# Kernel optimization log

Measured on AMD Instinct MI355X. Metric: run time of the kernel, lower is better.

The kernel has to match this reference:

```python
import math
import jax, jax.numpy as jnp
import numpy as np

FACTOR = 5
N_HEADS = 8


def setup_inputs() -> dict:
    key = jax.random.key(0)
    ks = jax.random.split(key, 9)
    B, S, D = 4, 8192, 512
    s = 0.02
    x = jax.random.normal(ks[0], (B, S, D), jnp.float32)
    Wq = jax.random.normal(ks[1], (D, D), jnp.float32) * s
    bq = jax.random.normal(ks[2], (D,), jnp.float32) * s
    Wk = jax.random.normal(ks[3], (D, D), jnp.float32) * s
    bk = jax.random.normal(ks[4], (D,), jnp.float32) * s
    Wv = jax.random.normal(ks[5], (D, D), jnp.float32) * s
    bv = jax.random.normal(ks[6], (D,), jnp.float32) * s
    Wo = jax.random.normal(ks[7], (D, D), jnp.float32) * s
    bo = jax.random.normal(ks[8], (D,), jnp.float32) * s
    return {"x": x, "Wq": Wq, "bq": bq, "Wk": Wk, "bk": bk,
            "Wv": Wv, "bv": bv, "Wo": Wo, "bo": bo}


def reference(x, Wq, bq, Wk, bk, Wv, bv, Wo, bo):
    B, S, D = x.shape
    H = N_HEADS
    hd = D // H
    scale = hd ** -0.5

    def proj(W, b):
        # [B,S,D] -> [B,H,S,hd]
        return (x @ W + b).reshape(B, S, H, hd).transpose(0, 2, 1, 3)

    q = proj(Wq, bq)
    k = proj(Wk, bk)
    v = proj(Wv, bv)

    # number of "active" queries: O(log S)
    sampled = max(1, min(S, int(FACTOR * math.log(S + 1))))

    sparsity = jnp.sum(q * q, axis=-1)                    # [B,H,S]
    top_idx = jax.lax.top_k(sparsity, sampled)[1]         # [B,H,u]

    sel_q = jnp.take_along_axis(q, top_idx[..., None], axis=2)  # [B,H,u,hd]
    scores = jnp.einsum('bhud,bhsd->bhus', sel_q, k) * scale     # [B,H,u,S]
    attn = jax.nn.softmax(scores, axis=-1)
    sel_ctx = jnp.einsum('bhus,bhsd->bhud', attn, v)             # [B,H,u,hd]

    # default context = mean of values; overwrite rows of selected queries
    ctx = jnp.broadcast_to(v.mean(axis=2, keepdims=True), (B, H, S, hd))
    bi = jnp.arange(B)[:, None, None]
    hi = jnp.arange(H)[None, :, None]
    ctx = ctx.at[bi, hi, top_idx].set(sel_ctx)                   # scatter [B,H,S,hd]

    ctx = ctx.transpose(0, 2, 1, 3).reshape(B, S, D)
    return ctx @ Wo + bo
```

## Files before the change

### kernel.cpp

```cpp
#include <hip/hip_runtime.h>
#include <hip/hip_fp16.h>
#include <math.h>

#define B_ 4
#define S_ 8192
#define D_ 512
#define H_ 8
#define U_ 45
#define NCHUNK 32

typedef unsigned short ushortT;
typedef __attribute__((ext_vector_type(8))) _Float16 half8;
typedef __attribute__((ext_vector_type(4))) float f32x4;

__device__ __forceinline__ ushortT f2h(float f) {
    return __half_as_ushort(__float2half(f));
}
__device__ __forceinline__ float h2f(ushortT u) {
    return __half2float(__ushort_as_half(u));
}

__device__ __forceinline__ void gload_lds16(const ushortT* g, ushortT* l) {
    __builtin_amdgcn_global_load_lds(
        (const __attribute__((address_space(1))) void*)g,
        (__attribute__((address_space(3))) void*)l,
        16, 0, 0);
}

__global__ __launch_bounds__(256) void prep_kernel(
    const float* __restrict__ X, ushortT* __restrict__ Xf,
    const float* __restrict__ Wq, const float* __restrict__ Wk,
    const float* __restrict__ Wv,
    ushortT* __restrict__ WqT, ushortT* __restrict__ WkT,
    ushortT* __restrict__ WvT,
    float* __restrict__ vsum, float* __restrict__ outbase)
{
    __shared__ float t[32][33];
    const int bx = blockIdx.x;
    if (bx < 8192) {
        if (bx == 0) {
            float4 z = {0.f, 0.f, 0.f, 0.f};
            *(float4*)&vsum[threadIdx.x * 8]        = z;
            *(float4*)&vsum[threadIdx.x * 8 + 4]    = z;
            *(float4*)&outbase[threadIdx.x * 8]     = z;
            *(float4*)&outbase[threadIdx.x * 8 + 4] = z;
        }
        size_t i = ((size_t)bx * 256 + threadIdx.x) * 8;
        float4 a = *(const float4*)(X + i);
        float4 b = *(const float4*)(X + i + 4);
        *(ushort4*)(Xf + i)     = make_ushort4(f2h(a.x), f2h(a.y), f2h(a.z), f2h(a.w));
        *(ushort4*)(Xf + i + 4) = make_ushort4(f2h(b.x), f2h(b.y), f2h(b.z), f2h(b.w));
    } else {
        const int idx = bx - 8192;
        const int z = idx >> 8, rem = idx & 255;
        const int r0 = (rem >> 4) * 32, c0 = (rem & 15) * 32;
        const float* W = (z == 0) ? Wq : (z == 1) ? Wk : Wv;
        ushortT* O = (z == 0) ? WqT : (z == 1) ? WkT : WvT;
        const int tx = threadIdx.x & 31, ty4 = (threadIdx.x >> 5) * 4;
#pragma unroll
        for (int i = 0; i < 4; ++i)
            t[ty4 + i][tx] = W[(size_t)(r0 + ty4 + i) * 512 + c0 + tx];
        __syncthreads();
#pragma unroll
        for (int i = 0; i < 4; ++i)
            O[(size_t)(c0 + ty4 + i) * 512 + r0 + tx] = f2h(t[tx][ty4 + i]);
    }
}

__global__ __launch_bounds__(512, 2) void qkv_mfma(
    const ushortT* __restrict__ Xf,
    const ushortT* __restrict__ WqT, const ushortT* __restrict__ WkT,
    const ushortT* __restrict__ WvT,
    const float* __restrict__ bq, const float* __restrict__ bk,
    const float* __restrict__ bv,
    ushortT* __restrict__ Kbuf, ushortT* __restrict__ VT,
    float* __restrict__ sparsity, float* __restrict__ vsum)
{
    __shared__ ushortT lds[3 * 128 * 64];

    const int tid  = threadIdx.x;
    const int w    = tid >> 6, lane = tid & 63;
    const int quad = lane >> 4, c16 = lane & 15;
    const bool fusedQK = (blockIdx.y < 4);
    const int stream = w >> 2;
    const int aw   = fusedQK ? ((w >> 1) & 1) : (w >> 1);
    const int bw   = w & 1;
    const int m0   = blockIdx.x * 128;
    const int n0   = fusedQK ? (blockIdx.y * 128) : ((blockIdx.y - 4) * 256);

    const int srowL = lane >> 3;
    const int slc   = (((lane & 7) - (srowL & 7)) & 7) * 8;
    const int rrot  = c16 & 7;

    const ushortT* Brd = fusedQK ? (lds + 8192 + stream * 8192) : (lds + 16384);
    const int awBase = aw * 64;
    const int bwBase = bw * 64;

    f32x4 acc[4][4];
#pragma unroll
    for (int i = 0; i < 4; ++i)
#pragma unroll
        for (int j = 0; j < 4; ++j) acc[i][j] = (f32x4){0.f, 0.f, 0.f, 0.f};

    for (int k0 = 0; k0 < 512; k0 += 64) {
        __syncthreads();
        if (fusedQK) {
#pragma unroll
            for (int c = 0; c < 2; ++c) {
                const int R  = c * 64 + w * 8 + srowL;
                const int lb = c * 4096 + w * 512;
                gload_lds16(Xf  + (size_t)(m0 + R) * 512 + k0 + slc, lds + lb);
                gload_lds16(WqT + (size_t)(n0 + R) * 512 + k0 + slc, lds + 8192 + lb);
                gload_lds16(WkT + (size_t)(n0 + R) * 512 + k0 + slc, lds + 16384 + lb);
            }
        } else {
#pragma unroll
            for (int c = 0; c < 4; ++c) {
                const int R = c * 64 + w * 8 + srowL;
                gload_lds16(WvT + (size_t)(n0 + R) * 512 + k0 + slc,
                            lds + c * 4096 + w * 512);
            }
#pragma unroll
            for (int c = 0; c < 2; ++c) {
                const int R = c * 64 + w * 8 + srowL;
                gload_lds16(Xf + (size_t)(m0 + R) * 512 + k0 + slc,
                            lds + 16384 + c * 4096 + w * 512);
            }
        }
        __syncthreads();
#pragma unroll
        for (int kk = 0; kk < 2; ++kk) {
            const int phk = (((kk * 4 + quad) + rrot) & 7) * 8;
            half8 af[4], bf[4];
#pragma unroll
            for (int i = 0; i < 4; ++i) {
                af[i] = *(const half8*)&lds[(awBase + i * 16 + c16) * 64 + phk];
                bf[i] = *(const half8*)&Brd[(bwBase + i * 16 + c16) * 64 + phk];
            }
#pragma unroll
            for (int i = 0; i < 4; ++i)
#pragma unroll
                for (int j = 0; j < 4; ++j)
                    acc[i][j] = __builtin_amdgcn_mfma_f32_16x16x32_f16(af[i], bf[j], acc[i][j], 0, 0, 0);
        }
    }

    const int b = m0 >> 13;
    if (fusedQK && stream == 0) {
        const int head = (n0 + bw * 64) >> 6;
        float bb[4];
#pragma unroll
        for (int j = 0; j < 4; ++j) bb[j] = bq[n0 + bw * 64 + j * 16 + c16];
#pragma unroll
        for (int i = 0; i < 4; ++i)
#pragma unroll
            for (int r = 0; r < 4; ++r) {
                const int s = (m0 & 8191) + awBase + i * 16 + quad * 4 + r;
                float p = 0.f;
#pragma unroll
                for (int j = 0; j < 4; ++j) {
                    float v = acc[i][j][r] + bb[j];
                    p = fmaf(v, v, p);
                }
                p += __shfl_xor(p, 1);
                p += __shfl_xor(p, 2);
                p += __shfl_xor(p, 4);
                p += __shfl_xor(p, 8);
                if (c16 == 0)
                    sparsity[((size_t)b * H_ + head) * S_ + s] = p;
            }
    } else if (fusedQK) {
        const int head = (n0 + bw * 64) >> 6;
        float bb[4];
#pragma unroll
        for (int j = 0; j < 4; ++j) bb[j] = bk[n0 + bw * 64 + j * 16 + c16];
        ushortT* kbase = Kbuf + ((size_t)(b * 8 + head) * 8192) * 64;
#pragma unroll
        for (int i = 0; i < 4; ++i)
#pragma unroll
            for (int r = 0; r < 4; ++r) {
                const int s = (m0 & 8191) + awBase + i * 16 + quad * 4 + r;
#pragma unroll
                for (int j = 0; j < 4; ++j)
                    kbase[(size_t)s * 64 + j * 16 + c16] = f2h(acc[i][j][r] + bb[j]);
            }
    } else {
        const int sbase = (m0 & 8191) + bwBase;
#pragma unroll
        for (int i = 0; i < 4; ++i)
#pragma unroll
            for (int r = 0; r < 4; ++r) {
                const int dcol = n0 + awBase + i * 16 + quad * 4 + r;
                const int head = dcol >> 6, dd = dcol & 63;
                const float biasv = bv[dcol];
                ushortT* vrow = VT + ((size_t)(b * 8 + head) * 64 + dd) * 8192;
                float vsa = 0.f;
#pragma unroll
                for (int j = 0; j < 4; ++j) {
                    float v = acc[i][j][r] + biasv;
                    vrow[sbase + j * 16 + c16] = f2h(v);
                    vsa += v;
                }
                vsa += __shfl_xor(vsa, 1);
                vsa += __shfl_xor(vsa, 2);
                vsa += __shfl_xor(vsa, 4);
                vsa += __shfl_xor(vsa, 8);
                if (c16 == 0) atomicAdd(&vsum[b * 512 + dcol], vsa);
            }
    }
}

__global__ __launch_bounds__(256) void topk_kernel(
    const float* __restrict__ sparsity, int* __restrict__ topidx,
    const float* __restrict__ vsum, const float* __restrict__ Wo,
    const float* __restrict__ bo, float* __restrict__ outbase,
    const ushortT* __restrict__ Xf, const ushortT* __restrict__ WqT,
    const float* __restrict__ bq, ushortT* __restrict__ selQ)
{
    __shared__ __align__(16) char smem[49920];
    unsigned* vals        = (unsigned*)smem;
    unsigned (*hist)[256] = (unsigned (*)[256])(smem + 32768);
    int* ssum             = (int*)(smem + 40960);
    int* eqidx            = (int*)(smem + 41984);
    ushortT* selX         = (ushortT*)smem;
    __shared__ unsigned prefix_s;
    __shared__ int need_s;
    __shared__ int cnt_gt_s, cnt_eq_s;
    const int tid = threadIdx.x;

    if (blockIdx.x >= 32) {
        const int idx = blockIdx.x - 32;
        const int b = idx >> 3, ks = (idx & 7) >> 1, dh = idx & 1;
        const int d = dh * 256 + tid;
        float acc = (ks == 0) ? bo[d] : 0.f;
        const int r0 = ks * 128;
        for (int r = r0; r < r0 + 128; ++r) {
            float mv = vsum[b * 512 + r] * (1.0f / S_);
            acc = fmaf(mv, Wo[(size_t)r * 512 + d], acc);
        }
        atomicAdd(&outbase[b * 512 + d], acc);
        return;
    }

    const int bh = blockIdx.x;
    const unsigned* sp = (const unsigned*)(sparsity + (size_t)bh * S_);
    for (int i = tid; i < S_; i += 256) vals[i] = sp[i];

    unsigned prefix = 0;
    int need = U_;
    const int rep = tid & 7;
    for (int level = 0; level < 4; ++level) {
        const int shift = 24 - level * 8;
#pragma unroll
        for (int r = 0; r < 8; ++r) hist[r][tid] = 0;
        __syncthreads();
        const unsigned pmask = (level == 0) ? 0u : (0xFFFFFFFFu << (shift + 8));
        for (int i = tid; i < S_; i += 256) {
            unsigned v = vals[i];
            if ((v & pmask) == prefix)
                atomicAdd(&hist[rep][(v >> shift) & 255], 1u);
        }
        __syncthreads();
        int bs = 0;
#pragma unroll
        for (int r = 0; r < 8; ++r) bs += (int)hist[r][tid];
        ssum[tid] = bs;
        __syncthreads();
        for (int off = 1; off < 256; off <<= 1) {
            int add = (tid + off < 256) ? ssum[tid + off] : 0;
            __syncthreads();
            ssum[tid] += add;
            __syncthreads();
        }
        int snext = (tid == 255) ? 0 : ssum[tid + 1];
        if (ssum[tid] >= need && snext < need) {
            prefix_s = prefix | ((unsigned)tid << shift);
            need_s = need - snext;
        }
        __syncthreads();
        prefix = prefix_s;
        need = need_s;
        __syncthreads();
    }
    const unsigned T = prefix;
    if (tid == 0) { cnt_gt_s = 0; cnt_eq_s = 0; }
    __syncthreads();
    for (int i = tid; i < S_; i += 256) {
        unsigned v = vals[i];
        if (v > T) {
            int p = atomicAdd(&cnt_gt_s, 1);
            topidx[bh * U_ + p] = i;
        } else if (v == T) {
            int p = atomicAdd(&cnt_eq_s, 1);
            if (p < 64) eqidx[p] = i;
        }
    }
    __syncthreads();
    if (tid == 0) {
        int rem = U_ - cnt_gt_s;
        int n = cnt_eq_s < 64 ? cnt_eq_s : 64;
        for (int a = 0; a < rem; ++a) {
            int best = 1 << 30, bj = 0;
            for (int j = 0; j < n; ++j)
                if (eqidx[j] < best) { best = eqidx[j]; bj = j; }
            topidx[bh * U_ + cnt_gt_s + a] = best;
            eqidx[bj] = 1 << 30;
        }
    }
    __syncthreads();

    const int b = bh >> 3, h = bh & 7;
    for (int i = tid; i < 48 * 64; i += 256) {
        const int row = i >> 6, ch = i & 63;
        half8 v;
#pragma unroll
        for (int z = 0; z < 8; ++z) v[z] = (_Float16)0.0f;
        if (row < U_) {
            const int s = topidx[bh * U_ + row];
            v = *(const half8*)&Xf[((size_t)b * 8192 + s) * 512 + ch * 8];
        }
        *(half8*)&selX[row * 520 + ch * 8] = v;
    }
    __syncthreads();

    const int w = tid >> 6, lane = tid & 63;
    const int quad = lane >> 4, c16 = lane & 15;
    f32x4 qacc[3];
#pragma unroll
    for (int mt = 0; mt < 3; ++mt) qacc[mt] = (f32x4){0.f, 0.f, 0.f, 0.f};
    const ushortT* brow = WqT + (size_t)(h * 64 + w * 16 + c16) * 512;
    for (int k0 = 0; k0 < 512; k0 += 32) {
        half8 bf = *(const half8*)&brow[k0 + quad * 8];
#pragma unroll
        for (int mt = 0; mt < 3; ++mt) {
            half8 af = *(const half8*)&selX[(mt * 16 + c16) * 520 + k0 + quad * 8];
            qacc[mt] = __builtin_amdgcn_mfma_f32_16x16x32_f16(af, bf, qacc[mt], 0, 0, 0);
        }
    }
    const float bb = bq[h * 64 + w * 16 + c16];
    ushortT* oq = selQ + (size_t)bh * 48 * 64 + (w * 16 + c16);
#pragma unroll
    for (int mt = 0; mt < 3; ++mt)
#pragma unroll
        for (int r = 0; r < 4; ++r) {
            const int m = mt * 16 + quad * 4 + r;
            float v = (m < U_) ? (qacc[mt][r] + bb) * 0.125f : 0.f;
            oq[(size_t)m * 64] = f2h(v);
        }
}

__global__ __launch_bounds__(256, 2) void attn_mfma(
    const ushortT* __restrict__ selQ, const ushortT* __restrict__ Kbuf,
    const ushortT* __restrict__ VT,
    float* __restrict__ pl, float* __restrict__ pacc)
{
    __shared__ float sc[48 * 132];

    const int tid = threadIdx.x;
    const int w = tid >> 6, lane = tid & 63;
    const int quad = lane >> 4, c16 = lane & 15;
    const int bh = blockIdx.y;
    const int s_base = blockIdx.x * (S_ / NCHUNK);

    f32x4 O[3];
#pragma unroll
    for (int mt = 0; mt < 3; ++mt) O[mt] = (f32x4){0.f, 0.f, 0.f, 0.f};
    float lacc[12];
#pragma unroll
    for (int qi = 0; qi < 12; ++qi) lacc[qi] = 0.f;

    const ushortT* sq = selQ + (size_t)bh * 48 * 64;
    half8 qa[3][2];
#pragma unroll
    for (int mt = 0; mt < 3; ++mt)
#pragma unroll
        for (int kk = 0; kk < 2; ++kk)
            qa[mt][kk] = *(const half8*)&sq[(mt * 16 + c16) * 64 + kk * 32 + quad * 8];

    const ushortT* kb  = Kbuf + (size_t)bh * 8192 * 64;
    const ushortT* vtb = VT + ((size_t)bh * 64 + w * 16 + c16) * 8192;

    half8 kf0[2][2], kf1[2][2], vb0[4], vb1[4];
#pragma unroll
    for (int nt2 = 0; nt2 < 2; ++nt2)
#pragma unroll
        for (int kk = 0; kk < 2; ++kk) {
            kf0[nt2][kk] = *(const half8*)&kb[
                (size_t)(s_base + w * 32 + nt2 * 16 + c16) * 64 + kk * 32 + quad * 8];
            kf1[nt2][kk] = *(const half8*)&kb[
                (size_t)(s_base + 128 + w * 32 + nt2 * 16 + c16) * 64 + kk * 32 + quad * 8];
        }
#pragma unroll
    for (int kk = 0; kk < 4; ++kk) {
        vb0[kk] = *(const half8*)&vtb[s_base + kk * 32 + quad * 8];
        vb1[kk] = *(const half8*)&vtb[s_base + 128 + kk * 32 + quad * 8];
    }

    auto chunk = [&](const half8 (&kf)[2][2], const half8 (&vb)[4]) {
        f32x4 sacc[3][2];
#pragma unroll
        for (int mt = 0; mt < 3; ++mt)
#pragma unroll
            for (int nt2 = 0; nt2 < 2; ++nt2) {
                sacc[mt][nt2] = (f32x4){0.f, 0.f, 0.f, 0.f};
#pragma unroll
                for (int kk = 0; kk < 2; ++kk)
                    sacc[mt][nt2] = __builtin_amdgcn_mfma_f32_16x16x32_f16(
                        qa[mt][kk], kf[nt2][kk], sacc[mt][nt2], 0, 0, 0);
            }
#pragma unroll
        for (int mt = 0; mt < 3; ++mt)
#pragma unroll
            for (int nt2 = 0; nt2 < 2; ++nt2)
#pragma unroll
                for (int r = 0; r < 4; ++r)
                    sc[(mt * 16 + quad * 4 + r) * 132 + w * 32 + nt2 * 16 + c16] =
                        sacc[mt][nt2][r];
        __syncthreads();

#pragma unroll
        for (int qi = 0; qi < 12; ++qi) {
            const int q = w * 12 + qi;
            float x0 = sc[q * 132 + lane];
            float x1 = sc[q * 132 + 64 + lane];
            ushortT u0 = f2h(__expf(x0));
            ushortT u1 = f2h(__expf(x1));
            lacc[qi] += h2f(u0) + h2f(u1);
            ushortT* pr = (ushortT*)&sc[q * 132];
            pr[lane] = u0;
            pr[lane + 64] = u1;
        }
        __syncthreads();

#pragma unroll
        for (int mt = 0; mt < 3; ++mt)
#pragma unroll
            for (int kk = 0; kk < 4; ++kk) {
                half8 pa = *(const half8*)((const ushortT*)sc +
                    (size_t)(mt * 16 + c16) * 264 + kk * 32 + quad * 8);
                O[mt] = __builtin_amdgcn_mfma_f32_16x16x32_f16(pa, vb[kk], O[mt], 0, 0, 0);
            }
        __syncthreads();
    };

    chunk(kf0, vb0);
    chunk(kf1, vb1);

#pragma unroll
    for (int mt = 0; mt < 3; ++mt)
#pragma unroll
        for (int r = 0; r < 4; ++r) {
            const int q = mt * 16 + quad * 4 + r;
            if (q < U_)
                pacc[(((size_t)bh * NCHUNK + blockIdx.x) * U_ + q) * 64 + w * 16 + c16] =
                    O[mt][r];
        }
#pragma unroll
    for (int qi = 0; qi < 12; ++qi) {
        const int q = w * 12 + qi;
        float ssum = lacc[qi];
#pragma unroll
        for (int off = 1; off < 64; off <<= 1) ssum += __shfl_xor(ssum, off);
        if (lane == 0 && q < U_)
            pl[((size_t)bh * NCHUNK + blockIdx.x) * U_ + q] = ssum;
    }
}

__global__ __launch_bounds__(256) void fill_kernel(
    const float* __restrict__ outbase, float* __restrict__ out)
{
    size_t gid = (size_t)blockIdx.x * 256 + threadIdx.x;
    size_t e0 = gid * 4;
    int b = (int)(e0 >> 22);
    int col = (int)(e0 & 511);
    float4 v = *(const float4*)&outbase[b * 512 + col];
    *(float4*)&out[e0] = v;
}

__global__ __launch_bounds__(512) void corr_out_kernel(
    const float* __restrict__ pl, const float* __restrict__ pacc,
    const float* __restrict__ vsum, const float* __restrict__ Wo,
    const int* __restrict__ topidx, float* __restrict__ out)
{
    __shared__ float redA[8][64];
    __shared__ float redL[8];
    __shared__ float corrS[64];
    const int q = blockIdx.x, bh = blockIdx.y;
    const int b = bh >> 3, h = bh & 7, tid = threadIdx.x;
    const int g = tid >> 6, lane = tid & 63;

    float a = 0.f, L = 0.f;
    for (int c = g; c < NCHUNK; c += 8) {
        a += pacc[(((size_t)bh * NCHUNK + c) * U_ + q) * 64 + lane];
        if (lane == 0) L += pl[((size_t)bh * NCHUNK + c) * U_ + q];
    }
    redA[g][lane] = a;
    if (lane == 0) redL[g] = L;
    __syncthreads();
    if (tid < 64) {
        float asum = 0.f, Lsum = 0.f;
#pragma unroll
        for (int gg = 0; gg < 8; ++gg) { asum += redA[gg][tid]; Lsum += redL[gg]; }
        corrS[tid] = asum / Lsum - vsum[b * 512 + h * 64 + tid] * (1.0f / S_);
    }
    __syncthreads();
    const int s = topidx[bh * U_ + q];
    const int d = tid;
    float delta = 0.f;
#pragma unroll
    for (int r = 0; r < 64; ++r)
        delta = fmaf(corrS[r], Wo[(size_t)(h * 64 + r) * 512 + d], delta);
    atomicAdd(&out[((size_t)b * S_ + s) * 512 + d], delta);
}

extern "C" void kernel_launch(void* const* d_in, const int* in_sizes, int n_in,
                              void* d_out, int out_size, void* d_ws, size_t ws_size,
                              hipStream_t stream)
{
    const float* X  = (const float*)d_in[0];
    const float* Wq = (const float*)d_in[1];
    const float* bq = (const float*)d_in[2];
    const float* Wk = (const float*)d_in[3];
    const float* bk = (const float*)d_in[4];
    const float* Wv = (const float*)d_in[5];
    const float* bv = (const float*)d_in[6];
    const float* Wo = (const float*)d_in[7];
    const float* bo = (const float*)d_in[8];
    float* out = (float*)d_out;

    char* ws = (char*)d_ws;
    size_t off = 0;
    auto alloc = [&](size_t bytes) {
        void* p = ws + off;
        off = (off + bytes + 255) & ~(size_t)255;
        return p;
    };
    ushortT* Xf   = (ushortT*)alloc((size_t)B_ * S_ * D_ * 2);
    ushortT* Kbuf = (ushortT*)alloc((size_t)B_ * S_ * D_ * 2);
    ushortT* VT   = (ushortT*)alloc((size_t)B_ * S_ * D_ * 2);
    ushortT* WqT  = (ushortT*)alloc((size_t)D_ * D_ * 2);
    ushortT* WkT  = (ushortT*)alloc((size_t)D_ * D_ * 2);
    ushortT* WvT  = (ushortT*)alloc((size_t)D_ * D_ * 2);
    ushortT* selQ = (ushortT*)alloc((size_t)B_ * H_ * 48 * 64 * 2);
    float* sparsity = (float*)alloc((size_t)B_ * H_ * S_ * 4);
    int*   topidx   = (int*)alloc((size_t)B_ * H_ * U_ * 4);
    float* pl       = (float*)alloc((size_t)B_ * H_ * NCHUNK * U_ * 4);
    float* pacc     = (float*)alloc((size_t)B_ * H_ * NCHUNK * U_ * 64 * 4);
    float* vsum     = (float*)alloc((size_t)B_ * 512 * 4);
    float* outbase  = (float*)alloc((size_t)B_ * 512 * 4);

    prep_kernel<<<8960, 256, 0, stream>>>(X, Xf, Wq, Wk, Wv, WqT, WkT, WvT,
                                          vsum, outbase);
    qkv_mfma<<<dim3(256, 6), 512, 0, stream>>>(Xf, WqT, WkT, WvT,
                                               bq, bk, bv, Kbuf, VT,
                                               sparsity, vsum);
    topk_kernel<<<64, 256, 0, stream>>>(sparsity, topidx, vsum, Wo, bo, outbase,
                                        Xf, WqT, bq, selQ);
    attn_mfma<<<dim3(NCHUNK, B_ * H_), 256, 0, stream>>>(selQ, Kbuf, VT,
                                                         pl, pacc);
    fill_kernel<<<(B_ * S_ * D_ / 4 + 255) / 256, 256, 0, stream>>>(outbase, out);
    corr_out_kernel<<<dim3(U_, B_ * H_), 512, 0, stream>>>(pl, pacc, vsum, Wo,
                                                           topidx, out);
}
```

Baseline: 277.2 us.

## Share X tile across Q and K accumulators in fused QK projection blocks

Fused Q/K blocks now cover 256 rows of X, and each wave keeps both Q and K accumulators, so one A-fragment load feeds two MFMAs. Before, Q and K were handled by separate wave groups that each re-read the same X tile. The grid is unchanged, so half of the QK blocks exit at once. Register pressure doubles to two 4x4 accumulator sets per wave, and LDS grows to four tiles, which may lower occupancy and cause spills under launch_bounds(512,2).

```diff
diff --git a/kernel.cpp b/kernel.cpp
--- a/kernel.cpp
+++ b/kernel.cpp
@@ -76,91 +76,89 @@
     ushortT* __restrict__ Kbuf, ushortT* __restrict__ VT,
     float* __restrict__ sparsity, float* __restrict__ vsum)
 {
-    __shared__ ushortT lds[3 * 128 * 64];
+    __shared__ ushortT lds[4 * 128 * 64];
 
     const int tid  = threadIdx.x;
     const int w    = tid >> 6, lane = tid & 63;
     const int quad = lane >> 4, c16 = lane & 15;
     const bool fusedQK = (blockIdx.y < 4);
-    const int stream = w >> 2;
-    const int aw   = fusedQK ? ((w >> 1) & 1) : (w >> 1);
-    const int bw   = w & 1;
-    const int m0   = blockIdx.x * 128;
-    const int n0   = fusedQK ? (blockIdx.y * 128) : ((blockIdx.y - 4) * 256);
-
     const int srowL = lane >> 3;
     const int slc   = (((lane & 7) - (srowL & 7)) & 7) * 8;
     const int rrot  = c16 & 7;
 
-    const ushortT* Brd = fusedQK ? (lds + 8192 + stream * 8192) : (lds + 16384);
-    const int awBase = aw * 64;
-    const int bwBase = bw * 64;
-
-    f32x4 acc[4][4];
-#pragma unroll
-    for (int i = 0; i < 4; ++i)
-#pragma unroll
-        for (int j = 0; j < 4; ++j) acc[i][j] = (f32x4){0.f, 0.f, 0.f, 0.f};
-
-    for (int k0 = 0; k0 < 512; k0 += 64) {
-        __syncthreads();
-        if (fusedQK) {
+    if (fusedQK) {
+        if (blockIdx.x >= 128) return;
+        const int m0 = blockIdx.x * 256;
+        const int n0 = blockIdx.y * 128;
+        const int wr = w >> 1, wc = w & 1;
+
+        f32x4 accQ[4][4], accK[4][4];
+#pragma unroll
+        for (int i = 0; i < 4; ++i)
+#pragma unroll
+            for (int j = 0; j < 4; ++j) {
+                accQ[i][j] = (f32x4){0.f, 0.f, 0.f, 0.f};
+                accK[i][j] = (f32x4){0.f, 0.f, 0.f, 0.f};
+            }
+
+        for (int k0 = 0; k0 < 512; k0 += 64) {
+            __syncthreads();
+#pragma unroll
+            for (int c = 0; c < 4; ++c) {
+                const int R = c * 64 + w * 8 + srowL;
+                gload_lds16(Xf + (size_t)(m0 + R) * 512 + k0 + slc,
+                            lds + c * 4096 + w * 512);
+            }
 #pragma unroll
             for (int c = 0; c < 2; ++c) {
                 const int R  = c * 64 + w * 8 + srowL;
                 const int lb = c * 4096 + w * 512;
-                gload_lds16(Xf  + (size_t)(m0 + R) * 512 + k0 + slc, lds + lb);
-                gload_lds16(WqT + (size_t)(n0 + R) * 512 + k0 + slc, lds + 8192 + lb);
-                gload_lds16(WkT + (size_t)(n0 + R) * 512 + k0 + slc, lds + 16384 + lb);
-            }
-        } else {
-#pragma unroll
-            for (int c = 0; c < 4; ++c) {
-                const int R = c * 64 + w * 8 + srowL;
-                gload_lds16(WvT + (size_t)(n0 + R) * 512 + k0 + slc,
-                            lds + c * 4096 + w * 512);
-            }
-#pragma unroll
-            for (int c = 0; c < 2; ++c) {
-                const int R = c * 64 + w * 8 + srowL;
-                gload_lds16(Xf + (size_t)(m0 + R) * 512 + k0 + slc,
-                            lds + 16384 + c * 4096 + w * 512);
-            }
-        }
-        __syncthreads();
-#pragma unroll
-        for (int kk = 0; kk < 2; ++kk) {
-            const int phk = (((kk * 4 + quad) + rrot) & 7) * 8;
-            half8 af[4], bf[4];
-#pragma unroll
-            for (int i = 0; i < 4; ++i) {
-                af[i] = *(const half8*)&lds[(awBase + i * 16 + c16) * 64 + phk];
-                bf[i] = *(const half8*)&Brd[(bwBase + i * 16 + c16) * 64 + phk];
-            }
-#pragma unroll
-            for (int i = 0; i < 4; ++i)
-#pragma unroll
-                for (int j = 0; j < 4; ++j)
-                    acc[i][j] = __builtin_amdgcn_mfma_f32_16x16x32_f16(af[i], bf[j], acc[i][j], 0, 0, 0);
-        }
-    }
-
-    const int b = m0 >> 13;
-    if (fusedQK && stream == 0) {
-        const int head = (n0 + bw * 64) >> 6;
-        float bb[4];
-#pragma unroll
-        for (int j = 0; j < 4; ++j) bb[j] = bq[n0 + bw * 64 + j * 16 + c16];
+                gload_lds16(WqT + (size_t)(n0 + R) * 512 + k0 + slc,
+                            lds + 16384 + lb);
+                gload_lds16(WkT + (size_t)(n0 + R) * 512 + k0 + slc,
+                            lds + 24576 + lb);
+            }
+            __syncthreads();
+#pragma unroll
+            for (int kk = 0; kk < 2; ++kk) {
+                const int phk = (((kk * 4 + quad) + rrot) & 7) * 8;
+                half8 af[4], bq8[4], bk8[4];
+#pragma unroll
+                for (int i = 0; i < 4; ++i) {
+                    af[i]  = *(const half8*)&lds[(wr * 64 + i * 16 + c16) * 64 + phk];
+                    bq8[i] = *(const half8*)&lds[16384 + (wc * 64 + i * 16 + c16) * 64 + phk];
+                    bk8[i] = *(const half8*)&lds[24576 + (wc * 64 + i * 16 + c16) * 64 + phk];
+                }
+#pragma unroll
+                for (int i = 0; i < 4; ++i)
+#pragma unroll
+                    for (int j = 0; j < 4; ++j) {
+                        accQ[i][j] = __builtin_amdgcn_mfma_f32_16x16x32_f16(af[i], bq8[j], accQ[i][j], 0, 0, 0);
+                        accK[i][j] = __builtin_amdgcn_mfma_f32_16x16x32_f16(af[i], bk8[j], accK[i][j], 0, 0, 0);
+                    }
+            }
+        }
+
+        const int b = m0 >> 13;
+        const int head = (n0 + wc * 64) >> 6;
+        float bbq[4], bbk[4];
+#pragma unroll
+        for (int j = 0; j < 4; ++j) {
+            bbq[j] = bq[n0 + wc * 64 + j * 16 + c16];
+            bbk[j] = bk[n0 + wc * 64 + j * 16 + c16];
+        }
+        ushortT* kbase = Kbuf + ((size_t)(b * 8 + head) * 8192) * 64;
 #pragma unroll
         for (int i = 0; i < 4; ++i)
 #pragma unroll
             for (int r = 0; r < 4; ++r) {
-                const int s = (m0 & 8191) + awBase + i * 16 + quad * 4 + r;
+                const int s = (m0 & 8191) + wr * 64 + i * 16 + quad * 4 + r;
                 float p = 0.f;
 #pragma unroll
                 for (int j = 0; j < 4; ++j) {
-                    float v = acc[i][j][r] + bb[j];
+                    float v = accQ[i][j][r] + bbq[j];
                     p = fmaf(v, v, p);
+                    kbase[(size_t)s * 64 + j * 16 + c16] = f2h(accK[i][j][r] + bbk[j]);
                 }
                 p += __shfl_xor(p, 1);
                 p += __shfl_xor(p, 2);
@@ -169,45 +167,78 @@
                 if (c16 == 0)
                     sparsity[((size_t)b * H_ + head) * S_ + s] = p;
             }
-    } else if (fusedQK) {
-        const int head = (n0 + bw * 64) >> 6;
-        float bb[4];
-#pragma unroll
-        for (int j = 0; j < 4; ++j) bb[j] = bk[n0 + bw * 64 + j * 16 + c16];
-        ushortT* kbase = Kbuf + ((size_t)(b * 8 + head) * 8192) * 64;
-#pragma unroll
-        for (int i = 0; i < 4; ++i)
-#pragma unroll
-            for (int r = 0; r < 4; ++r) {
-                const int s = (m0 & 8191) + awBase + i * 16 + quad * 4 + r;
+        return;
+    }
+
+    const int aw   = w >> 1;
+    const int bw   = w & 1;
+    const int m0   = blockIdx.x * 128;
+    const int n0   = (blockIdx.y - 4) * 256;
+    const ushortT* Brd = lds + 16384;
+    const int awBase = aw * 64;
+    const int bwBase = bw * 64;
+
+    f32x4 acc[4][4];
+#pragma unroll
+    for (int i = 0; i < 4; ++i)
+#pragma unroll
+        for (int j = 0; j < 4; ++j) acc[i][j] = (f32x4){0.f, 0.f, 0.f, 0.f};
+
+    for (int k0 = 0; k0 < 512; k0 += 64) {
+        __syncthreads();
+#pragma unroll
+        for (int c = 0; c < 4; ++c) {
+            const int R = c * 64 + w * 8 + srowL;
+            gload_lds16(WvT + (size_t)(n0 + R) * 512 + k0 + slc,
+                        lds + c * 4096 + w * 512);
+        }
+#pragma unroll
+        for (int c = 0; c < 2; ++c) {
+            const int R = c * 64 + w * 8 + srowL;
+            gload_lds16(Xf + (size_t)(m0 + R) * 512 + k0 + slc,
+                        lds + 16384 + c * 4096 + w * 512);
+        }
+        __syncthreads();
+#pragma unroll
+        for (int kk = 0; kk < 2; ++kk) {
+            const int phk = (((kk * 4 + quad) + rrot) & 7) * 8;
+            half8 af[4], bf[4];
+#pragma unroll
+            for (int i = 0; i < 4; ++i) {
+                af[i] = *(const half8*)&lds[(awBase + i * 16 + c16) * 64 + phk];
+                bf[i] = *(const half8*)&Brd[(bwBase + i * 16 + c16) * 64 + phk];
+            }
+#pragma unroll
+            for (int i = 0; i < 4; ++i)
 #pragma unroll
                 for (int j = 0; j < 4; ++j)
-                    kbase[(size_t)s * 64 + j * 16 + c16] = f2h(acc[i][j][r] + bb[j]);
-            }
-    } else {
-        const int sbase = (m0 & 8191) + bwBase;
-#pragma unroll
-        for (int i = 0; i < 4; ++i)
-#pragma unroll
-            for (int r = 0; r < 4; ++r) {
-                const int dcol = n0 + awBase + i * 16 + quad * 4 + r;
-                const int head = dcol >> 6, dd = dcol & 63;
-                const float biasv = bv[dcol];
-                ushortT* vrow = VT + ((size_t)(b * 8 + head) * 64 + dd) * 8192;
-                float vsa = 0.f;
-#pragma unroll
-                for (int j = 0; j < 4; ++j) {
-                    float v = acc[i][j][r] + biasv;
-                    vrow[sbase + j * 16 + c16] = f2h(v);
-                    vsa += v;
-                }
-                vsa += __shfl_xor(vsa, 1);
-                vsa += __shfl_xor(vsa, 2);
-                vsa += __shfl_xor(vsa, 4);
-                vsa += __shfl_xor(vsa, 8);
-                if (c16 == 0) atomicAdd(&vsum[b * 512 + dcol], vsa);
-            }
-    }
+                    acc[i][j] = __builtin_amdgcn_mfma_f32_16x16x32_f16(af[i], bf[j], acc[i][j], 0, 0, 0);
+        }
+    }
+
+    const int b = m0 >> 13;
+    const int sbase = (m0 & 8191) + bwBase;
+#pragma unroll
+    for (int i = 0; i < 4; ++i)
+#pragma unroll
+        for (int r = 0; r < 4; ++r) {
+            const int dcol = n0 + awBase + i * 16 + quad * 4 + r;
+            const int head = dcol >> 6, dd = dcol & 63;
+            const float biasv = bv[dcol];
+            ushortT* vrow = VT + ((size_t)(b * 8 + head) * 64 + dd) * 8192;
+            float vsa = 0.f;
+#pragma unroll
+            for (int j = 0; j < 4; ++j) {
+                float v = acc[i][j][r] + biasv;
+                vrow[sbase + j * 16 + c16] = f2h(v);
+                vsa += v;
+            }
+            vsa += __shfl_xor(vsa, 1);
+            vsa += __shfl_xor(vsa, 2);
+            vsa += __shfl_xor(vsa, 4);
+            vsa += __shfl_xor(vsa, 8);
+            if (c16 == 0) atomicAdd(&vsum[b * 512 + dcol], vsa);
+        }
 }
 
 __global__ __launch_bounds__(256) void topk_kernel(
```

New measurement: 299.7 us. 8.1% more time.
